# Optimization experiments

Measured on AMD Instinct MI355X. Metric: run time of the kernel, lower is better.

Reference implementation:

```python
import jax, jax.numpy as jnp
import numpy as np

H = 8   # num_heads
K = 7   # kernel_size


def setup_inputs() -> dict:
    key = jax.random.key(0)
    k1, k2, k3 = jax.random.split(key, 3)
    T, B, C = 2048, 16, 512
    x = jax.random.normal(k1, (T, B, C), dtype=jnp.float32)
    query = jax.random.normal(k2, (T, B, C), dtype=jnp.float32)
    W = jax.random.normal(k3, (C, H * K), dtype=jnp.float32) * 0.02
    return {"x": x, "query": query, "W": W}


def reference(x, query, W):
    T, B, C = x.shape
    R = C // H
    # per-position, per-head kernel weights: Dense(H*K) on query, no bias
    weight = jnp.einsum('tbc,cn->tbn', query, W).reshape(T * B * H, K)
    weight = jax.nn.softmax(weight, axis=-1)  # weight_softmax=True; dropout rate 0 is identity
    # TF extract_patches with SAME padding along T: total pad K-1, more on the bottom
    pad_before = (K - 1) // 2
    pad_after = K - 1 - pad_before
    x_pad = jnp.pad(x, ((pad_before, pad_after), (0, 0), (0, 0)))
    idx = jnp.arange(T)[:, None] + jnp.arange(K)[None, :]  # (T, K)
    patches = x_pad[idx]                      # (T, K, B, C)
    patches = jnp.transpose(patches, (0, 2, 1, 3))  # (T, B, K, C): TF depth order is (k, c)
    # Faithful to the source: flat (K*C) axis reinterpreted as (H, R, K)
    x_unfold = patches.reshape(T * B * H, R, K)
    out = jnp.einsum('nrk,nk->nr', x_unfold, weight)  # batched tiny matmul
    return out.reshape(T, B, C)
```

## Files before the change

kernel.cpp:

```cpp
#include <hip/hip_runtime.h>

#define T_DIM 2048
#define B_DIM 16
#define C_DIM 512
#define NW 56

#define XS_BYTES (22 * 512 * 2)
#define WT_OFF   XS_BYTES
#define F_LDS    (XS_BYTES + 3584)

typedef __attribute__((ext_vector_type(8))) short short8;
typedef __attribute__((ext_vector_type(4))) float floatx4;

static __device__ __forceinline__ unsigned short f2bf(float x) {
    union { float f; unsigned u; } v; v.f = x;
    return (unsigned short)((v.u + 0x7FFFu + ((v.u >> 16) & 1u)) >> 16);
}
static __device__ __forceinline__ float bf_lo(unsigned u) {
    union { unsigned u; float f; } c; c.u = u << 16; return c.f;
}
static __device__ __forceinline__ float bf_hi(unsigned u) {
    union { unsigned u; float f; } c; c.u = u & 0xFFFF0000u; return c.f;
}
static __device__ __forceinline__ int swz(int a) { return a ^ ((a >> 3) & 0x70); }

__global__ __launch_bounds__(256)
void pack_w(const float* __restrict__ W, short8* __restrict__ Bg) {
    const int g  = blockIdx.x * 256 + threadIdx.x;
    const int ks = g >> 8;
    const int nt = (g >> 6) & 3;
    const int l  = g & 63;
    const int c  = l & 15;
    const int n  = nt * 14 + c;
    const int k0 = ks * 32 + ((l >> 4) & 3) * 8;
    short8 o;
#pragma unroll
    for (int j = 0; j < 8; ++j) {
        const float v = (c < 14) ? W[(size_t)(k0 + j) * NW + n] : 0.f;
        o[j] = (short)f2bf(v);
    }
    Bg[g] = o;
}

__global__ __launch_bounds__(256)
void fused1(const float* __restrict__ x, const float* __restrict__ q,
            const short8* __restrict__ Bg, float* __restrict__ out) {
    __shared__ __align__(16) char S[F_LDS];

    const int tid  = threadIdx.x;
    const int lane = tid & 63;
    const int wv   = tid >> 6;
    const int b    = blockIdx.x & 15;
    const int t0   = (blockIdx.x >> 4) * 16;

    const int rq = lane & 15;
    const int qq = lane >> 4;
    const float* qbase = q + ((size_t)(t0 + rq) * B_DIM + b) * C_DIM + qq * 8;
    floatx4 acc = (floatx4){0.f, 0.f, 0.f, 0.f};
#pragma unroll 4
    for (int ks = 0; ks < 16; ++ks) {
        const float4 f0 = *(const float4*)(qbase + ks * 32);
        const float4 f1 = *(const float4*)(qbase + ks * 32 + 4);
        const short8 bf = Bg[(ks * 4 + wv) * 64 + lane];
        short8 af;
        af[0] = (short)f2bf(f0.x); af[1] = (short)f2bf(f0.y);
        af[2] = (short)f2bf(f0.z); af[3] = (short)f2bf(f0.w);
        af[4] = (short)f2bf(f1.x); af[5] = (short)f2bf(f1.y);
        af[6] = (short)f2bf(f1.z); af[7] = (short)f2bf(f1.w);
        acc = __builtin_amdgcn_mfma_f32_16x16x32_bf16(af, bf, acc, 0, 0, 0);
    }

    const int c    = lane & 15;
    const int cb   = (c < 7) ? 0 : 7;
    const int sb   = (lane & 48) + cb;
    const int quad = lane >> 4;
    float* wt = (float*)(S + WT_OFF);
#pragma unroll
    for (int r = 0; r < 4; ++r) {
        const float a = acc[r];
        const float v0 = __shfl(a, sb + 0);
        const float v1 = __shfl(a, sb + 1);
        const float v2 = __shfl(a, sb + 2);
        const float v3 = __shfl(a, sb + 3);
        const float v4 = __shfl(a, sb + 4);
        const float v5 = __shfl(a, sb + 5);
        const float v6 = __shfl(a, sb + 6);
        const float mx = fmaxf(fmaxf(fmaxf(v0, v1), fmaxf(v2, v3)),
                               fmaxf(fmaxf(v4, v5), v6));
        const float sm = __expf(v0 - mx) + __expf(v1 - mx) + __expf(v2 - mx) +
                         __expf(v3 - mx) + __expf(v4 - mx) + __expf(v5 - mx) +
                         __expf(v6 - mx);
        const float w = __expf(a - mx) * (1.0f / sm);
        if (c < 14)
            wt[(quad * 4 + r) * NW + wv * 14 + c] = w;
    }

    __builtin_amdgcn_sched_barrier(0);

    char* XS = S;
#pragma unroll
    for (int j = 0; j < 11; ++j) {
        const int idx = tid + j * 256;
        const int i   = idx >> 7;
        const int cc  = (idx & 127) * 4;
        const int tp  = t0 + i - 3;
        float4 xv = make_float4(0.f, 0.f, 0.f, 0.f);
        if (tp >= 0 && tp < T_DIM)
            xv = *(const float4*)(x + ((size_t)tp * B_DIM + b) * C_DIM + cc);
        uint2 p;
        p.x = (unsigned)f2bf(xv.x) | ((unsigned)f2bf(xv.y) << 16);
        p.y = (unsigned)f2bf(xv.z) | ((unsigned)f2bf(xv.w) << 16);
        *(uint2*)(XS + swz(idx * 8)) = p;
    }

    __syncthreads();

    const int h = lane >> 3;
    const int base_b = lane * 112;
#pragma unroll
    for (int s = 0; s < 4; ++s) {
        const int tt = wv * 4 + s;
        const int tb = tt * 1024 + base_b;
        uint4 xu[7];
#pragma unroll
        for (int i = 0; i < 7; ++i)
            xu[i] = *(const uint4*)(XS + swz(tb + i * 16));
        float xf[56];
#pragma unroll
        for (int i = 0; i < 7; ++i) {
            xf[i * 8 + 0] = bf_lo(xu[i].x); xf[i * 8 + 1] = bf_hi(xu[i].x);
            xf[i * 8 + 2] = bf_lo(xu[i].y); xf[i * 8 + 3] = bf_hi(xu[i].y);
            xf[i * 8 + 4] = bf_lo(xu[i].z); xf[i * 8 + 5] = bf_hi(xu[i].z);
            xf[i * 8 + 6] = bf_lo(xu[i].w); xf[i * 8 + 7] = bf_hi(xu[i].w);
        }
        const float* wp = wt + tt * NW + h * 7;
        float w[7];
#pragma unroll
        for (int k = 0; k < 7; ++k) w[k] = wp[k];
        float a8[8];
#pragma unroll
        for (int r = 0; r < 8; ++r) {
            float sacc = xf[r * 7] * w[0];
#pragma unroll
            for (int k = 1; k < 7; ++k) sacc = fmaf(w[k], xf[r * 7 + k], sacc);
            a8[r] = sacc;
        }
        float* orow = out + ((size_t)(t0 + tt) * B_DIM + b) * C_DIM + lane * 8;
        floatx4 v0 = (floatx4){a8[0], a8[1], a8[2], a8[3]};
        floatx4 v1 = (floatx4){a8[4], a8[5], a8[6], a8[7]};
        __builtin_nontemporal_store(v0, (floatx4*)orow);
        __builtin_nontemporal_store(v1, (floatx4*)(orow + 4));
    }
}

extern "C" void kernel_launch(void* const* d_in, const int* in_sizes, int n_in,
                              void* d_out, int out_size, void* d_ws, size_t ws_size,
                              hipStream_t stream) {
    const float* x = (const float*)d_in[0];
    const float* q = (const float*)d_in[1];
    const float* W = (const float*)d_in[2];
    float* out = (float*)d_out;
    short8* Bg = (short8*)d_ws;

    pack_w<<<16, 256, 0, stream>>>(W, Bg);
    fused1<<<(T_DIM / 16) * B_DIM, 256, 0, stream>>>(x, q, Bg, out);
}
```

Before: 201.2 us.

## Read x directly from global in a register double-buffered pipeline, halve block size

Drops the LDS staging of x, which was converted to bf16. Each thread now loads its fp32 unfold windows straight from global memory, double-buffered in registers, and computes 4 outputs per half-step. The block shrinks to 128 threads, each wave computing two MFMA n-tiles with the bf16 A fragments held in registers. A guarded path is kept only for the edge blocks. This removes LDS traffic and the bf16 rounding of x, in exchange for redundant global reads (each x row is read by up to seven neighbouring t positions, served by cache) and higher register pressure.

```diff
diff --git a/kernel.cpp b/kernel.cpp
--- a/kernel.cpp
+++ b/kernel.cpp
@@ -4,25 +4,15 @@
 #define B_DIM 16
 #define C_DIM 512
 #define NW 56
-
-#define XS_BYTES (22 * 512 * 2)
-#define WT_OFF   XS_BYTES
-#define F_LDS    (XS_BYTES + 3584)
+#define ROWSTEP (B_DIM * C_DIM)
 
 typedef __attribute__((ext_vector_type(8))) short short8;
 typedef __attribute__((ext_vector_type(4))) float floatx4;
 
-static __device__ __forceinline__ unsigned short f2bf(float x) {
-    union { float f; unsigned u; } v; v.f = x;
+static __device__ __forceinline__ unsigned short f2bf(float x_) {
+    union { float f; unsigned u; } v; v.f = x_;
     return (unsigned short)((v.u + 0x7FFFu + ((v.u >> 16) & 1u)) >> 16);
 }
-static __device__ __forceinline__ float bf_lo(unsigned u) {
-    union { unsigned u; float f; } c; c.u = u << 16; return c.f;
-}
-static __device__ __forceinline__ float bf_hi(unsigned u) {
-    union { unsigned u; float f; } c; c.u = u & 0xFFFF0000u; return c.f;
-}
-static __device__ __forceinline__ int swz(int a) { return a ^ ((a >> 3) & 0x70); }
 
 __global__ __launch_bounds__(256)
 void pack_w(const float* __restrict__ W, short8* __restrict__ Bg) {
@@ -42,115 +32,148 @@
     Bg[g] = o;
 }
 
-__global__ __launch_bounds__(256)
-void fused1(const float* __restrict__ x, const float* __restrict__ q,
+template<bool GUARD>
+static __device__ __forceinline__ void load_half(
+    float* pf, int m, const float* __restrict__ xb,
+    const float* __restrict__ x, int t0, int tbase, int b,
+    const int* offp, int lane) {
+    const int par = m & 1;
+    if (!GUARD) {
+        const float* bm = xb + (size_t)(m >> 1) * ROWSTEP;
+#pragma unroll
+        for (int j = 0; j < 7; ++j)
+            *(float4*)(pf + 4 * j) = *(const float4*)(bm + offp[par * 7 + j]);
+    } else {
+        const int tt = tbase + (m >> 1);
+#pragma unroll
+        for (int j = 0; j < 7; ++j) {
+            const int f  = 56 * lane + 28 * par + 4 * j;
+            const int kj = f >> 9;
+            const int cj = f & 511;
+            const int tp = t0 + tt + kj - 3;
+            const int tc = min(max(tp, 0), T_DIM - 1);
+            float4 v = *(const float4*)(x + ((size_t)tc * B_DIM + b) * C_DIM + cj);
+            if (tp < 0 || tp >= T_DIM) v = make_float4(0.f, 0.f, 0.f, 0.f);
+            *(float4*)(pf + 4 * j) = v;
+        }
+    }
+}
+
+static __device__ __forceinline__ void comp_half(
+    const float* pf, int m, int tbase, const float* wtl,
+    int t0, int b, float* __restrict__ out, int lane) {
+    const int par = m & 1, tt = tbase + (m >> 1);
+    const int h = lane >> 3;
+    const float* wrow = wtl + tt * NW + h * 7;
+    float wv[7];
+#pragma unroll
+    for (int k = 0; k < 7; ++k) wv[k] = wrow[k];
+    float a[4];
+#pragma unroll
+    for (int r = 0; r < 4; ++r) {
+        float s = pf[r * 7] * wv[0];
+#pragma unroll
+        for (int k = 1; k < 7; ++k) s = fmaf(wv[k], pf[r * 7 + k], s);
+        a[r] = s;
+    }
+    const floatx4 v = (floatx4){a[0], a[1], a[2], a[3]};
+    float* orow = out + ((size_t)(t0 + tt) * B_DIM + b) * C_DIM + lane * 8 + par * 4;
+    __builtin_nontemporal_store(v, (floatx4*)orow);
+}
+
+template<bool GUARD>
+static __device__ __forceinline__ void conv_pipeline(
+    const float* __restrict__ x, float* __restrict__ out,
+    const float* wtl, int t0, int b, int lane, int tbase) {
+    int offp[14];
+#pragma unroll
+    for (int par = 0; par < 2; ++par)
+#pragma unroll
+        for (int j = 0; j < 7; ++j) {
+            const int f = 56 * lane + 28 * par + 4 * j;
+            offp[par * 7 + j] = (f >> 9) * ROWSTEP + (f & 511);
+        }
+    const float* xb = x + ((ptrdiff_t)(t0 + tbase - 3) * B_DIM + b) * C_DIM;
+
+    float pA[28], pB[28];
+    load_half<GUARD>(pA, 0, xb, x, t0, tbase, b, offp, lane);
+    __syncthreads();
+#pragma unroll
+    for (int m = 0; m < 16; m += 2) {
+        load_half<GUARD>(pB, m + 1, xb, x, t0, tbase, b, offp, lane);
+        comp_half(pA, m, tbase, wtl, t0, b, out, lane);
+        if (m + 2 < 16)
+            load_half<GUARD>(pA, m + 2, xb, x, t0, tbase, b, offp, lane);
+        comp_half(pB, m + 1, tbase, wtl, t0, b, out, lane);
+    }
+}
+
+__global__ __launch_bounds__(128, 4)
+void fused2(const float* __restrict__ x, const float* __restrict__ q,
             const short8* __restrict__ Bg, float* __restrict__ out) {
-    __shared__ __align__(16) char S[F_LDS];
+    __shared__ __align__(16) float wtl[16 * NW];
 
     const int tid  = threadIdx.x;
     const int lane = tid & 63;
-    const int wv   = tid >> 6;
+    const int w    = tid >> 6;
     const int b    = blockIdx.x & 15;
     const int t0   = (blockIdx.x >> 4) * 16;
 
     const int rq = lane & 15;
     const int qq = lane >> 4;
     const float* qbase = q + ((size_t)(t0 + rq) * B_DIM + b) * C_DIM + qq * 8;
-    floatx4 acc = (floatx4){0.f, 0.f, 0.f, 0.f};
-#pragma unroll 4
+    short8 A[16];
+#pragma unroll
     for (int ks = 0; ks < 16; ++ks) {
         const float4 f0 = *(const float4*)(qbase + ks * 32);
         const float4 f1 = *(const float4*)(qbase + ks * 32 + 4);
-        const short8 bf = Bg[(ks * 4 + wv) * 64 + lane];
         short8 af;
         af[0] = (short)f2bf(f0.x); af[1] = (short)f2bf(f0.y);
         af[2] = (short)f2bf(f0.z); af[3] = (short)f2bf(f0.w);
         af[4] = (short)f2bf(f1.x); af[5] = (short)f2bf(f1.y);
         af[6] = (short)f2bf(f1.z); af[7] = (short)f2bf(f1.w);
-        acc = __builtin_amdgcn_mfma_f32_16x16x32_bf16(af, bf, acc, 0, 0, 0);
+        A[ks] = af;
     }
 
     const int c    = lane & 15;
     const int cb   = (c < 7) ? 0 : 7;
     const int sb   = (lane & 48) + cb;
     const int quad = lane >> 4;
-    float* wt = (float*)(S + WT_OFF);
 #pragma unroll
-    for (int r = 0; r < 4; ++r) {
-        const float a = acc[r];
-        const float v0 = __shfl(a, sb + 0);
-        const float v1 = __shfl(a, sb + 1);
-        const float v2 = __shfl(a, sb + 2);
-        const float v3 = __shfl(a, sb + 3);
-        const float v4 = __shfl(a, sb + 4);
-        const float v5 = __shfl(a, sb + 5);
-        const float v6 = __shfl(a, sb + 6);
-        const float mx = fmaxf(fmaxf(fmaxf(v0, v1), fmaxf(v2, v3)),
-                               fmaxf(fmaxf(v4, v5), v6));
-        const float sm = __expf(v0 - mx) + __expf(v1 - mx) + __expf(v2 - mx) +
-                         __expf(v3 - mx) + __expf(v4 - mx) + __expf(v5 - mx) +
-                         __expf(v6 - mx);
-        const float w = __expf(a - mx) * (1.0f / sm);
-        if (c < 14)
-            wt[(quad * 4 + r) * NW + wv * 14 + c] = w;
+    for (int ccn = 0; ccn < 2; ++ccn) {
+        const int nt = w * 2 + ccn;
+        floatx4 acc = (floatx4){0.f, 0.f, 0.f, 0.f};
+#pragma unroll 4
+        for (int ks = 0; ks < 16; ++ks) {
+            const short8 bf = Bg[(ks * 4 + nt) * 64 + lane];
+            acc = __builtin_amdgcn_mfma_f32_16x16x32_bf16(A[ks], bf, acc, 0, 0, 0);
+        }
+#pragma unroll
+        for (int r = 0; r < 4; ++r) {
+            const float a = acc[r];
+            const float v0 = __shfl(a, sb + 0);
+            const float v1 = __shfl(a, sb + 1);
+            const float v2 = __shfl(a, sb + 2);
+            const float v3 = __shfl(a, sb + 3);
+            const float v4 = __shfl(a, sb + 4);
+            const float v5 = __shfl(a, sb + 5);
+            const float v6 = __shfl(a, sb + 6);
+            const float mx = fmaxf(fmaxf(fmaxf(v0, v1), fmaxf(v2, v3)),
+                                   fmaxf(fmaxf(v4, v5), v6));
+            const float sm = __expf(v0 - mx) + __expf(v1 - mx) + __expf(v2 - mx) +
+                             __expf(v3 - mx) + __expf(v4 - mx) + __expf(v5 - mx) +
+                             __expf(v6 - mx);
+            const float wres = __expf(a - mx) * (1.0f / sm);
+            if (c < 14)
+                wtl[(quad * 4 + r) * NW + nt * 14 + c] = wres;
+        }
     }
 
-    __builtin_amdgcn_sched_barrier(0);
-
-    char* XS = S;
-#pragma unroll
-    for (int j = 0; j < 11; ++j) {
-        const int idx = tid + j * 256;
-        const int i   = idx >> 7;
-        const int cc  = (idx & 127) * 4;
-        const int tp  = t0 + i - 3;
-        float4 xv = make_float4(0.f, 0.f, 0.f, 0.f);
-        if (tp >= 0 && tp < T_DIM)
-            xv = *(const float4*)(x + ((size_t)tp * B_DIM + b) * C_DIM + cc);
-        uint2 p;
-        p.x = (unsigned)f2bf(xv.x) | ((unsigned)f2bf(xv.y) << 16);
-        p.y = (unsigned)f2bf(xv.z) | ((unsigned)f2bf(xv.w) << 16);
-        *(uint2*)(XS + swz(idx * 8)) = p;
-    }
-
-    __syncthreads();
-
-    const int h = lane >> 3;
-    const int base_b = lane * 112;
-#pragma unroll
-    for (int s = 0; s < 4; ++s) {
-        const int tt = wv * 4 + s;
-        const int tb = tt * 1024 + base_b;
-        uint4 xu[7];
-#pragma unroll
-        for (int i = 0; i < 7; ++i)
-            xu[i] = *(const uint4*)(XS + swz(tb + i * 16));
-        float xf[56];
-#pragma unroll
-        for (int i = 0; i < 7; ++i) {
-            xf[i * 8 + 0] = bf_lo(xu[i].x); xf[i * 8 + 1] = bf_hi(xu[i].x);
-            xf[i * 8 + 2] = bf_lo(xu[i].y); xf[i * 8 + 3] = bf_hi(xu[i].y);
-            xf[i * 8 + 4] = bf_lo(xu[i].z); xf[i * 8 + 5] = bf_hi(xu[i].z);
-            xf[i * 8 + 6] = bf_lo(xu[i].w); xf[i * 8 + 7] = bf_hi(xu[i].w);
-        }
-        const float* wp = wt + tt * NW + h * 7;
-        float w[7];
-#pragma unroll
-        for (int k = 0; k < 7; ++k) w[k] = wp[k];
-        float a8[8];
-#pragma unroll
-        for (int r = 0; r < 8; ++r) {
-            float sacc = xf[r * 7] * w[0];
-#pragma unroll
-            for (int k = 1; k < 7; ++k) sacc = fmaf(w[k], xf[r * 7 + k], sacc);
-            a8[r] = sacc;
-        }
-        float* orow = out + ((size_t)(t0 + tt) * B_DIM + b) * C_DIM + lane * 8;
-        floatx4 v0 = (floatx4){a8[0], a8[1], a8[2], a8[3]};
-        floatx4 v1 = (floatx4){a8[4], a8[5], a8[6], a8[7]};
-        __builtin_nontemporal_store(v0, (floatx4*)orow);
-        __builtin_nontemporal_store(v1, (floatx4*)(orow + 4));
-    }
+    const int tbase = w * 8;
+    if (t0 >= 16 && t0 <= T_DIM - 32)
+        conv_pipeline<false>(x, out, wtl, t0, b, lane, tbase);
+    else
+        conv_pipeline<true>(x, out, wtl, t0, b, lane, tbase);
 }
 
 extern "C" void kernel_launch(void* const* d_in, const int* in_sizes, int n_in,
@@ -163,5 +186,5 @@
     short8* Bg = (short8*)d_ws;
 
     pack_w<<<16, 256, 0, stream>>>(W, Bg);
-    fused1<<<(T_DIM / 16) * B_DIM, 256, 0, stream>>>(x, q, Bg, out);
+    fused2<<<(T_DIM / 16) * B_DIM, 128, 0, stream>>>(x, q, Bg, out);
 }
```

Result: slower. 268.4 us (+33.4%).

## Split fused kernel into separate weight-softmax and convolution kernels

Applied to the files above, without the earlier changes.

Breaks the single fused kernel into two: one computes the query projection and softmax weights and writes them to workspace, the other loads x and the precomputed weights and runs the dynamic convolution with 512-thread blocks. The weight kernel stages the bf16 query tile in LDS before the MFMA loop, and the conv kernel issues all global loads up front before converting. The aim is to let each phase reach better occupancy and memory-level parallelism. The cost is an extra launch and a round trip of the weights through global memory.

```diff
diff --git a/kernel.cpp b/kernel.cpp
--- a/kernel.cpp
+++ b/kernel.cpp
@@ -6,14 +6,14 @@
 #define NW 56
 
 #define XS_BYTES (22 * 512 * 2)
-#define WT_OFF   XS_BYTES
-#define F_LDS    (XS_BYTES + 3584)
+#define C_WT_OFF XS_BYTES
+#define C_LDS    (XS_BYTES + 3584)
 
 typedef __attribute__((ext_vector_type(8))) short short8;
 typedef __attribute__((ext_vector_type(4))) float floatx4;
 
-static __device__ __forceinline__ unsigned short f2bf(float x) {
-    union { float f; unsigned u; } v; v.f = x;
+static __device__ __forceinline__ unsigned short f2bf(float x_) {
+    union { float f; unsigned u; } v; v.f = x_;
     return (unsigned short)((v.u + 0x7FFFu + ((v.u >> 16) & 1u)) >> 16);
 }
 static __device__ __forceinline__ float bf_lo(unsigned u) {
@@ -43,9 +43,9 @@
 }
 
 __global__ __launch_bounds__(256)
-void fused1(const float* __restrict__ x, const float* __restrict__ q,
-            const short8* __restrict__ Bg, float* __restrict__ out) {
-    __shared__ __align__(16) char S[F_LDS];
+void weight2(const float* __restrict__ q, const short8* __restrict__ Bg,
+             float* __restrict__ wt_g) {
+    __shared__ __align__(16) short8 A8[16 * 64];
 
     const int tid  = threadIdx.x;
     const int lane = tid & 63;
@@ -55,26 +55,33 @@
 
     const int rq = lane & 15;
     const int qq = lane >> 4;
-    const float* qbase = q + ((size_t)(t0 + rq) * B_DIM + b) * C_DIM + qq * 8;
+    const float* qrow = q + ((size_t)(t0 + rq) * B_DIM + b) * C_DIM + qq * 8;
+#pragma unroll
+    for (int s = 0; s < 4; ++s) {
+        const int ks = wv + s * 4;
+        const float4 f0 = *(const float4*)(qrow + ks * 32);
+        const float4 f1 = *(const float4*)(qrow + ks * 32 + 4);
+        short8 o;
+        o[0] = (short)f2bf(f0.x); o[1] = (short)f2bf(f0.y);
+        o[2] = (short)f2bf(f0.z); o[3] = (short)f2bf(f0.w);
+        o[4] = (short)f2bf(f1.x); o[5] = (short)f2bf(f1.y);
+        o[6] = (short)f2bf(f1.z); o[7] = (short)f2bf(f1.w);
+        A8[ks * 64 + lane] = o;
+    }
+    __syncthreads();
+
     floatx4 acc = (floatx4){0.f, 0.f, 0.f, 0.f};
-#pragma unroll 4
+#pragma unroll
     for (int ks = 0; ks < 16; ++ks) {
-        const float4 f0 = *(const float4*)(qbase + ks * 32);
-        const float4 f1 = *(const float4*)(qbase + ks * 32 + 4);
         const short8 bf = Bg[(ks * 4 + wv) * 64 + lane];
-        short8 af;
-        af[0] = (short)f2bf(f0.x); af[1] = (short)f2bf(f0.y);
-        af[2] = (short)f2bf(f0.z); af[3] = (short)f2bf(f0.w);
-        af[4] = (short)f2bf(f1.x); af[5] = (short)f2bf(f1.y);
-        af[6] = (short)f2bf(f1.z); af[7] = (short)f2bf(f1.w);
-        acc = __builtin_amdgcn_mfma_f32_16x16x32_bf16(af, bf, acc, 0, 0, 0);
+        acc = __builtin_amdgcn_mfma_f32_16x16x32_bf16(A8[ks * 64 + lane], bf,
+                                                      acc, 0, 0, 0);
     }
 
     const int c    = lane & 15;
     const int cb   = (c < 7) ? 0 : 7;
     const int sb   = (lane & 48) + cb;
     const int quad = lane >> 4;
-    float* wt = (float*)(S + WT_OFF);
 #pragma unroll
     for (int r = 0; r < 4; ++r) {
         const float a = acc[r];
@@ -92,34 +99,61 @@
                          __expf(v6 - mx);
         const float w = __expf(a - mx) * (1.0f / sm);
         if (c < 14)
-            wt[(quad * 4 + r) * NW + wv * 14 + c] = w;
-    }
-
-    __builtin_amdgcn_sched_barrier(0);
+            wt_g[((size_t)(t0 + quad * 4 + r) * B_DIM + b) * NW + wv * 14 + c] = w;
+    }
+}
+
+__global__ __launch_bounds__(512)
+void conv2(const float* __restrict__ x, const float* __restrict__ wt_g,
+           float* __restrict__ out) {
+    __shared__ __align__(16) char S[C_LDS];
+
+    const int tid  = threadIdx.x;
+    const int lane = tid & 63;
+    const int wv   = tid >> 6;
+    const int b    = blockIdx.x & 15;
+    const int t0   = (blockIdx.x >> 4) * 16;
+
+    float4 xr[6];
+#pragma unroll
+    for (int j = 0; j < 6; ++j) {
+        const int idx = tid + j * 512;
+        xr[j] = make_float4(0.f, 0.f, 0.f, 0.f);
+        if (idx < 2816) {
+            const int i  = idx >> 7;
+            const int cc = (idx & 127) * 4;
+            const int tp = t0 + i - 3;
+            if (tp >= 0 && tp < T_DIM)
+                xr[j] = *(const float4*)(x + ((size_t)tp * B_DIM + b) * C_DIM + cc);
+        }
+    }
+    float4 wld = make_float4(0.f, 0.f, 0.f, 0.f);
+    const int wrow = tid / 14;
+    const int wj   = tid - wrow * 14;
+    if (tid < 224)
+        wld = *(const float4*)(wt_g + ((size_t)(t0 + wrow) * B_DIM + b) * NW + wj * 4);
 
     char* XS = S;
 #pragma unroll
-    for (int j = 0; j < 11; ++j) {
-        const int idx = tid + j * 256;
-        const int i   = idx >> 7;
-        const int cc  = (idx & 127) * 4;
-        const int tp  = t0 + i - 3;
-        float4 xv = make_float4(0.f, 0.f, 0.f, 0.f);
-        if (tp >= 0 && tp < T_DIM)
-            xv = *(const float4*)(x + ((size_t)tp * B_DIM + b) * C_DIM + cc);
-        uint2 p;
-        p.x = (unsigned)f2bf(xv.x) | ((unsigned)f2bf(xv.y) << 16);
-        p.y = (unsigned)f2bf(xv.z) | ((unsigned)f2bf(xv.w) << 16);
-        *(uint2*)(XS + swz(idx * 8)) = p;
-    }
-
+    for (int j = 0; j < 6; ++j) {
+        const int idx = tid + j * 512;
+        if (idx < 2816) {
+            uint2 p;
+            p.x = (unsigned)f2bf(xr[j].x) | ((unsigned)f2bf(xr[j].y) << 16);
+            p.y = (unsigned)f2bf(xr[j].z) | ((unsigned)f2bf(xr[j].w) << 16);
+            *(uint2*)(XS + swz(idx * 8)) = p;
+        }
+    }
+    if (tid < 224)
+        *(float4*)(S + C_WT_OFF + (wrow * NW + wj * 4) * 4) = wld;
     __syncthreads();
 
+    const float* wt = (const float*)(S + C_WT_OFF);
     const int h = lane >> 3;
     const int base_b = lane * 112;
 #pragma unroll
-    for (int s = 0; s < 4; ++s) {
-        const int tt = wv * 4 + s;
+    for (int s = 0; s < 2; ++s) {
+        const int tt = wv * 2 + s;
         const int tb = tt * 1024 + base_b;
         uint4 xu[7];
 #pragma unroll
@@ -146,8 +180,8 @@
             a8[r] = sacc;
         }
         float* orow = out + ((size_t)(t0 + tt) * B_DIM + b) * C_DIM + lane * 8;
-        floatx4 v0 = (floatx4){a8[0], a8[1], a8[2], a8[3]};
-        floatx4 v1 = (floatx4){a8[4], a8[5], a8[6], a8[7]};
+        const floatx4 v0 = (floatx4){a8[0], a8[1], a8[2], a8[3]};
+        const floatx4 v1 = (floatx4){a8[4], a8[5], a8[6], a8[7]};
         __builtin_nontemporal_store(v0, (floatx4*)orow);
         __builtin_nontemporal_store(v1, (floatx4*)(orow + 4));
     }
@@ -160,8 +194,10 @@
     const float* q = (const float*)d_in[1];
     const float* W = (const float*)d_in[2];
     float* out = (float*)d_out;
-    short8* Bg = (short8*)d_ws;
+    short8* Bg  = (short8*)d_ws;
+    float* wt_g = (float*)((char*)d_ws + 65536);
 
     pack_w<<<16, 256, 0, stream>>>(W, Bg);
-    fused1<<<(T_DIM / 16) * B_DIM, 256, 0, stream>>>(x, q, Bg, out);
-}
+    weight2<<<(T_DIM / 16) * B_DIM, 256, 0, stream>>>(q, Bg, wt_g);
+    conv2<<<(T_DIM / 16) * B_DIM, 512, 0, stream>>>(x, wt_g, out);
+}
```

Result: faster. 183.8 us (-8.7%).
